# Kernel optimization log

Measured on AMD Instinct MI355X. Metric: run time of the kernel, lower is better.

## Reference

```python
import jax, jax.numpy as jnp
import numpy as np

BSZ, SEQLEN, DIM = 2, 2048, 4096
N_HEADS, N_KV_HEADS, HEAD_DIM = 32, 8, 128
N_REP = N_HEADS // N_KV_HEADS
MAX_SEQ_LEN = 2048
ROPE_THETA = 500000.0
NEG_INF = -1e9


def setup_inputs() -> dict:
    key = jax.random.key(0)
    ks = jax.random.split(key, 6)
    scale = 0.02
    x = jax.random.normal(ks[0], (BSZ, SEQLEN, DIM), dtype=jnp.float32)
    wq = jax.random.normal(ks[1], (DIM, N_HEADS * HEAD_DIM), dtype=jnp.float32) * scale
    wk = jax.random.normal(ks[2], (DIM, N_KV_HEADS * HEAD_DIM), dtype=jnp.float32) * scale
    wv = jax.random.normal(ks[3], (DIM, N_KV_HEADS * HEAD_DIM), dtype=jnp.float32) * scale
    wo = jax.random.normal(ks[4], (N_HEADS * HEAD_DIM, DIM), dtype=jnp.float32) * scale
    # RoPE frequencies (llama precompute_freqs_cis)
    inv_freq = 1.0 / (ROPE_THETA ** (jnp.arange(0, HEAD_DIM, 2, dtype=jnp.float32) / HEAD_DIM))
    t = jnp.arange(SEQLEN, dtype=jnp.float32)
    freqs = jnp.outer(t, inv_freq)  # [seqlen, head_dim//2]
    freqs_cos = jnp.cos(freqs)
    freqs_sin = jnp.sin(freqs)
    # causal additive mask for prefill (start_pos=0)
    mask = jnp.triu(jnp.full((SEQLEN, SEQLEN), NEG_INF, dtype=jnp.float32), k=1)
    cache_k = jnp.zeros((BSZ, MAX_SEQ_LEN, N_KV_HEADS, HEAD_DIM), dtype=jnp.float32)
    cache_v = jnp.zeros((BSZ, MAX_SEQ_LEN, N_KV_HEADS, HEAD_DIM), dtype=jnp.float32)
    return {"x": x, "wq": wq, "wk": wk, "wv": wv, "wo": wo,
            "freqs_cos": freqs_cos, "freqs_sin": freqs_sin, "mask": mask,
            "cache_k": cache_k, "cache_v": cache_v, "start_pos": 0}


def apply_rotary_emb(x, cos, sin):
    # x: [b, s, h, d]; cos/sin: [s, d//2]
    x2 = x.reshape(*x.shape[:-1], -1, 2)
    xe, xo = x2[..., 0], x2[..., 1]
    c = cos[None, :, None, :]
    s = sin[None, :, None, :]
    oe = xe * c - xo * s
    oo = xe * s + xo * c
    return jnp.stack([oe, oo], axis=-1).reshape(x.shape)


def repeat_kv(x, n_rep):
    # [b, k, n_kv, d] -> [b, k, n_kv*n_rep, d]
    b, k, h, d = x.shape
    return jnp.broadcast_to(x[:, :, :, None, :], (b, k, h, n_rep, d)).reshape(b, k, h * n_rep, d)


def reference(x, wq, wk, wv, wo, freqs_cos, freqs_sin, mask, cache_k, cache_v, start_pos):
    bsz, seqlen, _ = x.shape
    xq = (x @ wq).reshape(bsz, seqlen, N_HEADS, HEAD_DIM)
    xk = (x @ wk).reshape(bsz, seqlen, N_KV_HEADS, HEAD_DIM)
    xv = (x @ wv).reshape(bsz, seqlen, N_KV_HEADS, HEAD_DIM)
    xq = apply_rotary_emb(xq, freqs_cos, freqs_sin)
    xk = apply_rotary_emb(xk, freqs_cos, freqs_sin)
    # KV-cache append
    cache_k = jax.lax.dynamic_update_slice(cache_k, xk, (0, start_pos, 0, 0))
    cache_v = jax.lax.dynamic_update_slice(cache_v, xv, (0, start_pos, 0, 0))
    kv_len = start_pos + seqlen
    keys = repeat_kv(cache_k[:, :kv_len], N_REP)      # [b, k, H, d]
    values = repeat_kv(cache_v[:, :kv_len], N_REP)
    q = xq.transpose(0, 2, 1, 3)                      # [b, H, s, d]
    k = keys.transpose(0, 2, 1, 3)
    v = values.transpose(0, 2, 1, 3)
    scores = jnp.einsum('bhsd,bhkd->bhsk', q, k) / jnp.sqrt(jnp.float32(HEAD_DIM))
    scores = scores + mask[None, None, :, :]
    probs = jax.nn.softmax(scores.astype(jnp.float32), axis=-1).astype(q.dtype)
    out = jnp.einsum('bhsk,bhkd->bhsd', probs, v)
    out = out.transpose(0, 2, 1, 3).reshape(bsz, seqlen, -1)
    return out @ wo
```

## Files before the change

kernel.cpp:

```cpp
#include <hip/hip_runtime.h>
#include <hip/hip_bf16.h>

typedef __bf16 bf16_t;
typedef __attribute__((ext_vector_type(4))) __bf16 bf16x4;
typedef __attribute__((ext_vector_type(8))) __bf16 bf16x8;
typedef __attribute__((ext_vector_type(4))) float f32x4;

#define DIM   4096
#define NQKV  6144
#define S_LEN 2048
#define HD    128

__device__ __forceinline__ void gload_lds16(const void* g, void* l) {
  __builtin_amdgcn_global_load_lds(
      (__attribute__((address_space(1))) void*)(g),
      (__attribute__((address_space(3))) void*)(l), 16, 0, 0);
}

__global__ __launch_bounds__(256) void convert_bf16(const float* __restrict__ src,
                                                    bf16_t* __restrict__ dst) {
  size_t i = ((size_t)blockIdx.x * 256 + threadIdx.x) * 8;
  f32x4 a = *(const f32x4*)(src + i);
  f32x4 b = *(const f32x4*)(src + i + 4);
  bf16x8 o;
#pragma unroll
  for (int j = 0; j < 4; ++j) { o[j] = (bf16_t)a[j]; o[4 + j] = (bf16_t)b[j]; }
  *(bf16x8*)(dst + i) = o;
}

__global__ __launch_bounds__(256) void transpose_conv(const float* __restrict__ src,
                                                      bf16_t* __restrict__ dst,
                                                      int K, int N) {
  __shared__ float tile[64][65];
  const int k0 = blockIdx.y * 64, n0 = blockIdx.x * 64;
  const int t = threadIdx.x;
#pragma unroll
  for (int p = 0; p < 4; ++p) {
    int idx = p * 256 + t;
    int r = idx >> 4, c4 = (idx & 15) * 4;
    f32x4 v = *(const f32x4*)&src[(size_t)(k0 + r) * N + n0 + c4];
    tile[r][c4] = v[0]; tile[r][c4 + 1] = v[1];
    tile[r][c4 + 2] = v[2]; tile[r][c4 + 3] = v[3];
  }
  __syncthreads();
#pragma unroll
  for (int p = 0; p < 4; ++p) {
    int idx = p * 256 + t;
    int r = idx >> 4, c4 = (idx & 15) * 4;
    bf16x4 o;
    o[0] = (bf16_t)tile[c4][r];     o[1] = (bf16_t)tile[c4 + 1][r];
    o[2] = (bf16_t)tile[c4 + 2][r]; o[3] = (bf16_t)tile[c4 + 3][r];
    *(bf16x4*)&dst[(size_t)(n0 + r) * K + k0 + c4] = o;
  }
}

template <typename CT, bool ROPE>
__global__ __launch_bounds__(512) void gemm256(const bf16_t* __restrict__ A,
                                               const bf16_t* __restrict__ Bt,
                                               CT* __restrict__ C,
                                               int N, int nbx,
                                               const float* __restrict__ cosT,
                                               const float* __restrict__ sinT) {
  __shared__ __align__(16) bf16_t As[32768];
  __shared__ __align__(16) bf16_t Bs[32768];
  const int tid  = threadIdx.x;
  const int lane = tid & 63;
  const int w    = tid >> 6;
  const int wm   = w >> 2, wn = w & 3;
  const int l15 = lane & 15, l4 = lane >> 4, l7 = lane & 7;

  const int cpx = gridDim.x >> 3;
  const int swz = (blockIdx.x & 7) * cpx + (blockIdx.x >> 3);
  const int by = swz / nbx, bx = swz - by * nbx;
  const int bm = by * 256, bn = bx * 256;

  const size_t g_off0 = (size_t)((w * 2 + 0) * 8 + (lane >> 3)) * 4096
                      + (((lane & 7) ^ ((lane >> 3) & 7)) * 8);
  const size_t g_off1 = g_off0 + (size_t)8 * 4096;
  const int l_off0 = (w * 2 + 0) * 512;
  const int l_off1 = (w * 2 + 1) * 512;

#define STAGE(gsrc, ldst) do { \
    gload_lds16((gsrc) + g_off0, (ldst) + l_off0); \
    gload_lds16((gsrc) + g_off1, (ldst) + l_off1); } while (0)

  const bf16_t* Ab = A  + (size_t)bm * 4096;
  const bf16_t* Bb = Bt + (size_t)bn * 4096;
  const size_t HLF = (size_t)128 * 4096;

  f32x4 acc[8][4];
#pragma unroll
  for (int i = 0; i < 8; ++i)
#pragma unroll
    for (int j = 0; j < 4; ++j) { f32x4 z = {0.f, 0.f, 0.f, 0.f}; acc[i][j] = z; }

  STAGE(Bb,             Bs);
  STAGE(Ab,             As);
  STAGE(Bb + HLF,       Bs + 8192);
  STAGE(Ab + HLF,       As + 8192);
  STAGE(Bb + 64,        Bs + 16384);
  STAGE(Ab + 64,        As + 16384);
  STAGE(Bb + HLF + 64,  Bs + 16384 + 8192);
  asm volatile("s_waitcnt vmcnt(6)" ::: "memory");
  __builtin_amdgcn_s_barrier();

  for (int t = 0; t < 64; ++t) {
    const int cu = t & 1;
    bf16_t* Ac = As + cu * 16384;
    bf16_t* Bc = Bs + cu * 16384;
    bf16_t* Axn = As + (cu ^ 1) * 16384;
    const bf16_t* A1g = Ab + (size_t)(t + 1) * 64;
    const bf16_t* A2g = Ab + (size_t)(t + 2) * 64;
    const bf16_t* B2g = Bb + (size_t)(t + 2) * 64;

    bf16x8 af[4][2], b0[2][2], b1[2][2];

#pragma unroll
    for (int f = 0; f < 4; ++f)
#pragma unroll
      for (int kh = 0; kh < 2; ++kh)
        af[f][kh] = *(const bf16x8*)&Ac[(wm * 64 + f * 16 + l15) * 64 + (((kh * 4 + l4) ^ l7) * 8)];
#pragma unroll
    for (int fb = 0; fb < 2; ++fb)
#pragma unroll
      for (int kh = 0; kh < 2; ++kh)
        b0[fb][kh] = *(const bf16x8*)&Bc[(wn * 32 + fb * 16 + l15) * 64 + (((kh * 4 + l4) ^ l7) * 8)];
    if (t + 1 < 64) STAGE(A1g + HLF, Axn + 8192);
    __builtin_amdgcn_s_barrier();
    asm volatile("s_waitcnt lgkmcnt(0)" ::: "memory");
    __builtin_amdgcn_sched_barrier(0);
    __builtin_amdgcn_s_setprio(1);
#pragma unroll
    for (int f = 0; f < 4; ++f)
#pragma unroll
      for (int fb = 0; fb < 2; ++fb)
#pragma unroll
        for (int kh = 0; kh < 2; ++kh)
          acc[f][fb] = __builtin_amdgcn_mfma_f32_16x16x32_bf16(af[f][kh], b0[fb][kh], acc[f][fb], 0, 0, 0);
    __builtin_amdgcn_s_setprio(0);
    __builtin_amdgcn_s_barrier();

#pragma unroll
    for (int fb = 0; fb < 2; ++fb)
#pragma unroll
      for (int kh = 0; kh < 2; ++kh)
        b1[fb][kh] = *(const bf16x8*)&Bc[8192 + (wn * 32 + fb * 16 + l15) * 64 + (((kh * 4 + l4) ^ l7) * 8)];
    if (t + 2 < 64) STAGE(B2g, Bc);
    __builtin_amdgcn_s_barrier();
    asm volatile("s_waitcnt lgkmcnt(0)" ::: "memory");
    __builtin_amdgcn_sched_barrier(0);
    __builtin_amdgcn_s_setprio(1);
#pragma unroll
    for (int f = 0; f < 4; ++f)
#pragma unroll
      for (int fb = 0; fb < 2; ++fb)
#pragma unroll
        for (int kh = 0; kh < 2; ++kh)
          acc[f][2 + fb] = __builtin_amdgcn_mfma_f32_16x16x32_bf16(af[f][kh], b1[fb][kh], acc[f][2 + fb], 0, 0, 0);
    __builtin_amdgcn_s_setprio(0);
    __builtin_amdgcn_s_barrier();

#pragma unroll
    for (int f = 0; f < 4; ++f)
#pragma unroll
      for (int kh = 0; kh < 2; ++kh)
        af[f][kh] = *(const bf16x8*)&Ac[8192 + (wm * 64 + f * 16 + l15) * 64 + (((kh * 4 + l4) ^ l7) * 8)];
    if (t + 2 < 64) STAGE(A2g, Ac);
    __builtin_amdgcn_s_barrier();
    asm volatile("s_waitcnt lgkmcnt(0)" ::: "memory");
    __builtin_amdgcn_sched_barrier(0);
    __builtin_amdgcn_s_setprio(1);
#pragma unroll
    for (int f = 0; f < 4; ++f)
#pragma unroll
      for (int fb = 0; fb < 2; ++fb)
#pragma unroll
        for (int kh = 0; kh < 2; ++kh)
          acc[4 + f][fb] = __builtin_amdgcn_mfma_f32_16x16x32_bf16(af[f][kh], b0[fb][kh], acc[4 + f][fb], 0, 0, 0);
    __builtin_amdgcn_s_setprio(0);
    __builtin_amdgcn_s_barrier();

    if (t + 2 < 64) STAGE(B2g + HLF, Bc + 8192);
    __builtin_amdgcn_s_barrier();
    __builtin_amdgcn_s_setprio(1);
#pragma unroll
    for (int f = 0; f < 4; ++f)
#pragma unroll
      for (int fb = 0; fb < 2; ++fb)
#pragma unroll
        for (int kh = 0; kh < 2; ++kh)
          acc[4 + f][2 + fb] = __builtin_amdgcn_mfma_f32_16x16x32_bf16(af[f][kh], b1[fb][kh], acc[4 + f][2 + fb], 0, 0, 0);
    __builtin_amdgcn_s_setprio(0);
    if (t < 62)       asm volatile("s_waitcnt vmcnt(6)" ::: "memory");
    else if (t == 62) asm volatile("s_waitcnt vmcnt(0)" ::: "memory");
    __builtin_amdgcn_s_barrier();
  }
#undef STAGE

#pragma unroll
  for (int mi = 0; mi < 8; ++mi) {
    int row0 = bm + (mi >> 2) * 128 + wm * 64 + (mi & 3) * 16 + l4 * 4;
#pragma unroll
    for (int ni = 0; ni < 4; ++ni) {
      int col = bn + (ni >> 1) * 128 + wn * 32 + (ni & 1) * 16 + l15;
      if (ROPE && col < 5120) {
        const int i = (col & 127) >> 1;
        const bool isq = (col < 4096);
        const float scl = isq ? 0.12751745f : 1.0f;
#pragma unroll
        for (int r = 0; r < 4; ++r) {
          int srow = (row0 + r) & (S_LEN - 1);
          float c = cosT[srow * 64 + i] * scl;
          float s = sinT[srow * 64 + i] * scl;
          float a = acc[mi][ni][r];
          float p = __shfl_xor(a, 1);
          float o = (l15 & 1) ? (p * s + a * c) : (a * c - p * s);
          C[(size_t)(row0 + r) * N + col] = (CT)o;
        }
      } else {
#pragma unroll
        for (int r = 0; r < 4; ++r)
          C[(size_t)(row0 + r) * N + col] = (CT)acc[mi][ni][r];
      }
    }
  }
}

__global__ __launch_bounds__(512) void attn_fwd(const bf16_t* __restrict__ qkv,
                                                bf16_t* __restrict__ out) {
  const int pr = blockIdx.x;
  const int h  = blockIdx.y;
  const int b  = blockIdx.z;
  const int kvh = h >> 2;
  const int tid = threadIdx.x;
  const int w    = tid >> 6;
  const int lane = tid & 63;
  const int qloc = lane & 15;
  const int g    = lane >> 4;

  __shared__ __align__(16) bf16_t Ks[2][64 * 128];
  __shared__ __align__(16) bf16_t Vt[128 * 64];

  const bf16_t* kvbase = qkv + (size_t)b * S_LEN * NQKV + DIM + kvh * HD;
  const int vrow_t = tid >> 4;
  const int vcol_t = (tid & 15) * 8;

  const float M2 = 11.5415603f;

#pragma unroll 1
  for (int half = 0; half < 2; ++half) {
    const int qt = half ? pr : 7 - pr;
    const int W = qt * 256 + w * 32;
    const int nt = 4 * qt + 4;

    bf16x8 aq[2][4];
#pragma unroll
    for (int qb = 0; qb < 2; ++qb) {
      const bf16_t* qptr = qkv + (size_t)(b * S_LEN + W + qb * 16 + qloc) * NQKV + h * HD + g * 8;
#pragma unroll
      for (int c = 0; c < 4; ++c) aq[qb][c] = *(const bf16x8*)(qptr + c * 32);
    }

    f32x4 oacc[2][8];
    float lsum[2] = {0.f, 0.f};
#pragma unroll
    for (int qb = 0; qb < 2; ++qb)
#pragma unroll
      for (int d = 0; d < 8; ++d) { f32x4 z = {0.f, 0.f, 0.f, 0.f}; oacc[qb][d] = z; }

    bf16x8 vreg[2];
#pragma unroll
    for (int p = 0; p < 2; ++p) {
      int chunk = p * 8 + w;
      int krow = chunk * 4 + g;
      int key = (krow & 3) | (((krow >> 3) & 1) << 2);
      gload_lds16(kvbase + (size_t)krow * NQKV + ((qloc ^ key) * 8), &Ks[0][chunk * 512]);
    }
#pragma unroll
    for (int p = 0; p < 2; ++p)
      vreg[p] = *(const bf16x8*)(kvbase + 1024 + (size_t)(p * 32 + vrow_t) * NQKV + vcol_t);

#pragma unroll 1
    for (int t = 0; t < nt; ++t) {
      const int kv0 = t * 64;
      const int cur = t & 1;

      if (t + 1 < nt) {
        const int kvn = kv0 + 64;
#pragma unroll
        for (int p = 0; p < 2; ++p) {
          int chunk = p * 8 + w;
          int krow = chunk * 4 + g;
          int key = (krow & 3) | (((krow >> 3) & 1) << 2);
          gload_lds16(kvbase + (size_t)(kvn + krow) * NQKV + ((qloc ^ key) * 8),
                      &Ks[cur ^ 1][chunk * 512]);
        }
        asm volatile("s_waitcnt vmcnt(2)" ::: "memory");
      } else {
        asm volatile("s_waitcnt vmcnt(0)" ::: "memory");
      }

#pragma unroll
      for (int p = 0; p < 2; ++p) {
        int vrow = p * 32 + vrow_t;
        int rk = (vrow >> 3) ^ (tid & 7);
#pragma unroll
        for (int j = 0; j < 8; ++j)
          Vt[(vcol_t + j) * 64 + ((rk ^ j) * 8) + (vrow & 7)] = vreg[p][j];
      }
      if (t + 1 < nt) {
        const int kvn = kv0 + 64;
#pragma unroll
        for (int p = 0; p < 2; ++p)
          vreg[p] = *(const bf16x8*)(kvbase + 1024 + (size_t)(kvn + p * 32 + vrow_t) * NQKV + vcol_t);
      }
      asm volatile("s_waitcnt lgkmcnt(0)" ::: "memory");
      __builtin_amdgcn_s_barrier();

      if (kv0 <= W + 31) {
        f32x4 sacc[2][2][2];
#pragma unroll
        for (int qb = 0; qb < 2; ++qb)
#pragma unroll
          for (int w2 = 0; w2 < 2; ++w2)
#pragma unroll
            for (int hf = 0; hf < 2; ++hf) { f32x4 z = {0.f, 0.f, 0.f, 0.f}; sacc[qb][w2][hf] = z; }
#pragma unroll
        for (int w2 = 0; w2 < 2; ++w2)
#pragma unroll
          for (int hf = 0; hf < 2; ++hf) {
            int r = 32 * w2 + 8 * (qloc >> 2) + 4 * hf + (qloc & 3);
            int key = (r & 3) | (((r >> 3) & 1) << 2);
            bf16x8 bk[4];
#pragma unroll
            for (int c = 0; c < 4; ++c)
              bk[c] = *(const bf16x8*)&Ks[cur][r * 128 + (((c * 4 + g) ^ key) * 8)];
            __builtin_amdgcn_s_setprio(1);
#pragma unroll
            for (int qb = 0; qb < 2; ++qb)
#pragma unroll
              for (int c = 0; c < 4; ++c)
                sacc[qb][w2][hf] = __builtin_amdgcn_mfma_f32_16x16x32_bf16(bk[c], aq[qb][c], sacc[qb][w2][hf], 0, 0, 0);
            __builtin_amdgcn_s_setprio(0);
          }

        const bool diag = (kv0 + 63 > W);
        bf16x8 pa[2][2];
#pragma unroll
        for (int qb = 0; qb < 2; ++qb) {
          const int qg = W + qb * 16 + qloc;
#pragma unroll
          for (int w2 = 0; w2 < 2; ++w2)
#pragma unroll
            for (int hf = 0; hf < 2; ++hf)
#pragma unroll
              for (int r = 0; r < 4; ++r) {
                float e = exp2f(sacc[qb][w2][hf][r] - M2);
                if (diag) {
                  int kg = kv0 + 32 * w2 + 8 * g + 4 * hf + r;
                  e = (kg <= qg) ? e : 0.f;
                }
                lsum[qb] += e;
                pa[qb][w2][hf * 4 + r] = (bf16_t)e;
              }
        }

#pragma unroll
        for (int w2 = 0; w2 < 2; ++w2)
#pragma unroll
          for (int dt = 0; dt < 8; ++dt) {
            int d = dt * 16 + qloc;
            int key2 = (4 * w2 + g) ^ (d & 7) ^ ((d >> 3) & 7);
            bf16x8 bv = *(const bf16x8*)&Vt[d * 64 + key2 * 8];
            __builtin_amdgcn_s_setprio(1);
#pragma unroll
            for (int qb = 0; qb < 2; ++qb)
              oacc[qb][dt] = __builtin_amdgcn_mfma_f32_16x16x32_bf16(bv, pa[qb][w2], oacc[qb][dt], 0, 0, 0);
            __builtin_amdgcn_s_setprio(0);
          }
      }
      __builtin_amdgcn_s_barrier();
    }

#pragma unroll
    for (int qb = 0; qb < 2; ++qb) {
      float ls = lsum[qb];
      ls += __shfl_xor(ls, 16);
      ls += __shfl_xor(ls, 32);
      float inv = 1.f / ls;
      bf16_t* op = out + (size_t)(b * S_LEN + W + qb * 16 + qloc) * DIM + h * HD;
#pragma unroll
      for (int dt = 0; dt < 8; ++dt) {
        bf16x4 o4;
#pragma unroll
        for (int r = 0; r < 4; ++r) o4[r] = (bf16_t)(oacc[qb][dt][r] * inv);
        *(bf16x4*)(op + dt * 16 + 4 * g) = o4;
      }
    }
  }
}

extern "C" void kernel_launch(void* const* d_in, const int* in_sizes, int n_in,
                              void* d_out, int out_size, void* d_ws, size_t ws_size,
                              hipStream_t stream) {
  const float* x  = (const float*)d_in[0];
  const float* wq = (const float*)d_in[1];
  const float* wk = (const float*)d_in[2];
  const float* wv = (const float*)d_in[3];
  const float* wo = (const float*)d_in[4];
  const float* fc = (const float*)d_in[5];
  const float* fs = (const float*)d_in[6];

  bf16_t* ws    = (bf16_t*)d_ws;
  bf16_t* wqkvT = ws;
  bf16_t* woT   = wqkvT + (size_t)6144 * 4096;
  bf16_t* qkv   = woT   + (size_t)4096 * 4096;
  bf16_t* xb    = qkv   + (size_t)4096 * 6144;
  bf16_t* ao    = xb;

  convert_bf16<<<8192, 256, 0, stream>>>(x, xb);
  transpose_conv<<<dim3(64, 64), 256, 0, stream>>>(wq, wqkvT, 4096, 4096);
  transpose_conv<<<dim3(16, 64), 256, 0, stream>>>(wk, wqkvT + (size_t)4096 * 4096, 4096, 1024);
  transpose_conv<<<dim3(16, 64), 256, 0, stream>>>(wv, wqkvT + (size_t)5120 * 4096, 4096, 1024);
  transpose_conv<<<dim3(64, 64), 256, 0, stream>>>(wo, woT, 4096, 4096);

  gemm256<bf16_t, true><<<384, 512, 0, stream>>>(xb, wqkvT, qkv, 6144, 24, fc, fs);
  attn_fwd<<<dim3(4, 32, 2), 512, 0, stream>>>(qkv, ao);
  gemm256<float, false><<<256, 512, 0, stream>>>(ao, woT, (float*)d_out, 4096, 16, nullptr, nullptr);
}
```

Before: 530.1 us.

## Split QKV GEMM into 256-tile Q part and 128x256-tile KV part

The fused QKV projection previously ran as 384 blocks of 256x256 tiles, which does not divide evenly over the CUs and leaves a partial second wave. It is now split into a Q GEMM with 256 blocks of 256x256 and a new KV GEMM kernel using 128x256 tiles, also 256 blocks, writing into the same output with a column offset. The intent is to reduce wave-quantization tail. The cost is two launches instead of one and a smaller-tile kernel with less data reuse per block.

Result: faster. 498.3 us (-6.0%).

```diff
diff --git a/kernel.cpp b/kernel.cpp
--- a/kernel.cpp
+++ b/kernel.cpp
@@ -58,7 +58,7 @@
 __global__ __launch_bounds__(512) void gemm256(const bf16_t* __restrict__ A,
                                                const bf16_t* __restrict__ Bt,
                                                CT* __restrict__ C,
-                                               int N, int nbx,
+                                               int ldc, int nbx, int col0,
                                                const float* __restrict__ cosT,
                                                const float* __restrict__ sinT) {
   __shared__ __align__(16) bf16_t As[32768];
@@ -203,10 +203,10 @@
 #pragma unroll
     for (int ni = 0; ni < 4; ++ni) {
       int col = bn + (ni >> 1) * 128 + wn * 32 + (ni & 1) * 16 + l15;
-      if (ROPE && col < 5120) {
-        const int i = (col & 127) >> 1;
-        const bool isq = (col < 4096);
-        const float scl = isq ? 0.12751745f : 1.0f;
+      int gcol = col0 + col;
+      if (ROPE && gcol < 5120) {
+        const int i = (gcol & 127) >> 1;
+        const float scl = (gcol < 4096) ? 0.12751745f : 1.0f;
 #pragma unroll
         for (int r = 0; r < 4; ++r) {
           int srow = (row0 + r) & (S_LEN - 1);
@@ -215,12 +215,148 @@
           float a = acc[mi][ni][r];
           float p = __shfl_xor(a, 1);
           float o = (l15 & 1) ? (p * s + a * c) : (a * c - p * s);
-          C[(size_t)(row0 + r) * N + col] = (CT)o;
+          C[(size_t)(row0 + r) * ldc + gcol] = (CT)o;
         }
       } else {
 #pragma unroll
         for (int r = 0; r < 4; ++r)
-          C[(size_t)(row0 + r) * N + col] = (CT)acc[mi][ni][r];
+          C[(size_t)(row0 + r) * ldc + gcol] = (CT)acc[mi][ni][r];
+      }
+    }
+  }
+}
+
+template <typename CT, bool ROPE>
+__global__ __launch_bounds__(512) void gemm128(const bf16_t* __restrict__ A,
+                                               const bf16_t* __restrict__ Bt,
+                                               CT* __restrict__ C,
+                                               int ldc, int nbx, int col0,
+                                               const float* __restrict__ cosT,
+                                               const float* __restrict__ sinT) {
+  __shared__ __align__(16) bf16_t As[2][8192];
+  __shared__ __align__(16) bf16_t Bs[2][16384];
+  const int tid  = threadIdx.x;
+  const int lane = tid & 63;
+  const int w    = tid >> 6;
+  const int wm   = w >> 2, wn = w & 3;
+  const int l15 = lane & 15, l4 = lane >> 4, l7 = lane & 7;
+
+  const int cpx = gridDim.x >> 3;
+  const int swz = (blockIdx.x & 7) * cpx + (blockIdx.x >> 3);
+  const int by = swz / nbx, bx = swz - by * nbx;
+  const int bm = by * 128, bn = bx * 256;
+
+  const size_t g_off0 = (size_t)((w * 2 + 0) * 8 + (lane >> 3)) * 4096
+                      + (((lane & 7) ^ ((lane >> 3) & 7)) * 8);
+  const size_t g_off1 = g_off0 + (size_t)8 * 4096;
+  const int l_off0 = (w * 2 + 0) * 512;
+  const int l_off1 = (w * 2 + 1) * 512;
+
+#define STAGE(gsrc, ldst) do { \
+    gload_lds16((gsrc) + g_off0, (ldst) + l_off0); \
+    gload_lds16((gsrc) + g_off1, (ldst) + l_off1); } while (0)
+
+  const bf16_t* Ab = A  + (size_t)bm * 4096;
+  const bf16_t* Bb = Bt + (size_t)bn * 4096;
+  const size_t HLF = (size_t)128 * 4096;
+
+  f32x4 acc[4][4];
+#pragma unroll
+  for (int i = 0; i < 4; ++i)
+#pragma unroll
+    for (int j = 0; j < 4; ++j) { f32x4 z = {0.f, 0.f, 0.f, 0.f}; acc[i][j] = z; }
+
+  STAGE(Ab,        &As[0][0]);
+  STAGE(Bb,        &Bs[0][0]);
+  STAGE(Bb + HLF,  &Bs[0][8192]);
+  STAGE(Bb + 64,   &Bs[1][0]);
+  asm volatile("s_waitcnt vmcnt(2)" ::: "memory");
+  __builtin_amdgcn_s_barrier();
+
+  for (int t = 0; t < 64; ++t) {
+    const int cu = t & 1;
+    const bf16_t* A1g = Ab + (size_t)(t + 1) * 64;
+    const bf16_t* B1g = Bb + (size_t)(t + 1) * 64;
+    const bf16_t* B2g = Bb + (size_t)(t + 2) * 64;
+
+    bf16x8 af[4][2], bl[2][2], bh[2][2];
+
+#pragma unroll
+    for (int f = 0; f < 4; ++f)
+#pragma unroll
+      for (int kh = 0; kh < 2; ++kh)
+        af[f][kh] = *(const bf16x8*)&As[cu][(wm * 64 + f * 16 + l15) * 64 + (((kh * 4 + l4) ^ l7) * 8)];
+#pragma unroll
+    for (int fb = 0; fb < 2; ++fb)
+#pragma unroll
+      for (int kh = 0; kh < 2; ++kh)
+        bl[fb][kh] = *(const bf16x8*)&Bs[cu][(wn * 32 + fb * 16 + l15) * 64 + (((kh * 4 + l4) ^ l7) * 8)];
+    if (t + 1 < 64) {
+      STAGE(A1g,       &As[cu ^ 1][0]);
+      STAGE(B1g + HLF, &Bs[cu ^ 1][8192]);
+    }
+    __builtin_amdgcn_s_barrier();
+    asm volatile("s_waitcnt lgkmcnt(0)" ::: "memory");
+    __builtin_amdgcn_sched_barrier(0);
+    __builtin_amdgcn_s_setprio(1);
+#pragma unroll
+    for (int f = 0; f < 4; ++f)
+#pragma unroll
+      for (int fb = 0; fb < 2; ++fb)
+#pragma unroll
+        for (int kh = 0; kh < 2; ++kh)
+          acc[f][fb] = __builtin_amdgcn_mfma_f32_16x16x32_bf16(af[f][kh], bl[fb][kh], acc[f][fb], 0, 0, 0);
+    __builtin_amdgcn_s_setprio(0);
+    __builtin_amdgcn_s_barrier();
+
+#pragma unroll
+    for (int fb = 0; fb < 2; ++fb)
+#pragma unroll
+      for (int kh = 0; kh < 2; ++kh)
+        bh[fb][kh] = *(const bf16x8*)&Bs[cu][8192 + (wn * 32 + fb * 16 + l15) * 64 + (((kh * 4 + l4) ^ l7) * 8)];
+    if (t + 2 < 64) STAGE(B2g, &Bs[cu][0]);
+    __builtin_amdgcn_s_barrier();
+    asm volatile("s_waitcnt lgkmcnt(0)" ::: "memory");
+    __builtin_amdgcn_sched_barrier(0);
+    __builtin_amdgcn_s_setprio(1);
+#pragma unroll
+    for (int f = 0; f < 4; ++f)
+#pragma unroll
+      for (int fb = 0; fb < 2; ++fb)
+#pragma unroll
+        for (int kh = 0; kh < 2; ++kh)
+          acc[f][2 + fb] = __builtin_amdgcn_mfma_f32_16x16x32_bf16(af[f][kh], bh[fb][kh], acc[f][2 + fb], 0, 0, 0);
+    __builtin_amdgcn_s_setprio(0);
+    if (t + 2 < 64) asm volatile("s_waitcnt vmcnt(2)" ::: "memory");
+    else            asm volatile("s_waitcnt vmcnt(0)" ::: "memory");
+    __builtin_amdgcn_s_barrier();
+  }
+#undef STAGE
+
+#pragma unroll
+  for (int f = 0; f < 4; ++f) {
+    int row0 = bm + wm * 64 + f * 16 + l4 * 4;
+#pragma unroll
+    for (int fb = 0; fb < 4; ++fb) {
+      int col = bn + (fb >> 1) * 128 + wn * 32 + (fb & 1) * 16 + l15;
+      int gcol = col0 + col;
+      if (ROPE && gcol < 5120) {
+        const int i = (gcol & 127) >> 1;
+        const float scl = (gcol < 4096) ? 0.12751745f : 1.0f;
+#pragma unroll
+        for (int r = 0; r < 4; ++r) {
+          int srow = (row0 + r) & (S_LEN - 1);
+          float c = cosT[srow * 64 + i] * scl;
+          float s = sinT[srow * 64 + i] * scl;
+          float a = acc[f][fb][r];
+          float p = __shfl_xor(a, 1);
+          float o = (l15 & 1) ? (p * s + a * c) : (a * c - p * s);
+          C[(size_t)(row0 + r) * ldc + gcol] = (CT)o;
+        }
+      } else {
+#pragma unroll
+        for (int r = 0; r < 4; ++r)
+          C[(size_t)(row0 + r) * ldc + gcol] = (CT)acc[f][fb][r];
       }
     }
   }
@@ -424,7 +560,9 @@
   transpose_conv<<<dim3(16, 64), 256, 0, stream>>>(wv, wqkvT + (size_t)5120 * 4096, 4096, 1024);
   transpose_conv<<<dim3(64, 64), 256, 0, stream>>>(wo, woT, 4096, 4096);
 
-  gemm256<bf16_t, true><<<384, 512, 0, stream>>>(xb, wqkvT, qkv, 6144, 24, fc, fs);
+  gemm256<bf16_t, true><<<256, 512, 0, stream>>>(xb, wqkvT, qkv, 6144, 16, 0, fc, fs);
+  gemm128<bf16_t, true><<<256, 512, 0, stream>>>(xb, wqkvT + (size_t)4096 * 4096, qkv,
+                                                 6144, 8, 4096, fc, fs);
   attn_fwd<<<dim3(4, 32, 2), 512, 0, stream>>>(qkv, ao);
-  gemm256<float, false><<<256, 512, 0, stream>>>(ao, woT, (float*)d_out, 4096, 16, nullptr, nullptr);
-}
+  gemm256<float, false><<<256, 512, 0, stream>>>(ao, woT, (float*)d_out, 4096, 16, 0, nullptr, nullptr);
+}
```
